# Kernel optimization log

Measured on AMD Instinct MI355X. Metric: run time of the kernel, lower is better.

The kernel has to match this reference:

```python
import jax, jax.numpy as jnp
import numpy as np

WIN_H, WIN_W = 4, 7
WIN = WIN_H * WIN_W  # 28 sample points == feature channels
GRID_OFF = (0.0, 40.0)
SPATIAL_SCALE = 1.0 / 0.4
BN_EPS = 1e-3


def setup_inputs() -> dict:
    key = jax.random.key(0)
    ks = jax.random.split(key, 5)
    B, Cin, H, W = 4, 256, 200, 176
    Cout, N = WIN, 2048
    x = jax.random.normal(ks[0], (B, Cin, H, W), dtype=jnp.float32)
    # boxes [x, y, z, w, l, h, r] in realistic KITTI ranges
    lo = jnp.array([0.0, -40.0, -3.0, 1.5, 3.2, 1.4, -np.pi], jnp.float32)
    hi = jnp.array([70.0, 40.0, 1.0, 2.0, 4.2, 1.8, np.pi], jnp.float32)
    u = jax.random.uniform(ks[1], (B, N, 7), dtype=jnp.float32)
    guided_anchors = lo + u * (hi - lo)
    w1 = jax.random.normal(ks[2], (Cout, Cin, 3, 3), jnp.float32) * 0.02
    gamma = jnp.ones((Cout,), jnp.float32)
    beta = jnp.zeros((Cout,), jnp.float32)
    running_mean = jnp.zeros((Cout,), jnp.float32)
    running_var = jnp.ones((Cout,), jnp.float32)
    w2 = jax.random.normal(ks[3], (Cout, Cout, 1, 1), jnp.float32) * 0.05
    return dict(x=x, guided_anchors=guided_anchors, w1=w1, gamma=gamma,
                beta=beta, running_mean=running_mean, running_var=running_var, w2=w2)


def _convs(x, w1, gamma, beta, mean, var, w2):
    dn = ('NCHW', 'OIHW', 'NCHW')
    y = jax.lax.conv_general_dilated(x, w1, (1, 1), 'SAME', dimension_numbers=dn)
    scale = gamma * jax.lax.rsqrt(var + BN_EPS)
    y = y * scale[:, None, None] + (beta - mean * scale)[:, None, None]  # BN (inference)
    y = jax.nn.relu(y)
    return jax.lax.conv_general_dilated(y, w2, (1, 1), 'SAME', dimension_numbers=dn)


def _gen_sample_grid(box5):
    xg, yg, wg, lg, rg = (box5[:, i] for i in range(5))
    c = jnp.cos(rg)[:, None, None]
    s = jnp.sin(rg)[:, None, None]
    xx = (jnp.linspace(-0.5, 0.5, WIN_H)[None, :] * wg[:, None])[:, :, None]  # (N,4,1)
    yy = (jnp.linspace(-0.5, 0.5, WIN_W)[None, :] * lg[:, None])[:, None, :]  # (N,1,7)
    xpix = xx * c + yy * s + xg[:, None, None]  # (N,4,7)
    ypix = yy * c - xx * s + yg[:, None, None]  # (N,4,7)
    xs = ((jnp.transpose(xpix, (1, 2, 0)) + GRID_OFF[0]) * SPATIAL_SCALE).reshape(WIN, -1)
    ys = ((jnp.transpose(ypix, (1, 2, 0)) + GRID_OFF[1]) * SPATIAL_SCALE).reshape(WIN, -1)
    return xs, ys


def _bilinear_sample(img, xs, ys):
    # img: (C,H,W); xs, ys: (C,N) pixel coords (align_corners=True semantics,
    # zero padding outside) -> (C,N). Channel c samples at grid row c.
    C, H, W = img.shape
    x0 = jnp.floor(xs); y0 = jnp.floor(ys)
    wx = xs - x0; wy = ys - y0
    cidx = jnp.arange(C)[:, None]

    def gather(yf, xf):
        yi = yf.astype(jnp.int32); xi = xf.astype(jnp.int32)
        valid = (yf >= 0) & (yf <= H - 1) & (xf >= 0) & (xf <= W - 1)
        v = img[cidx, jnp.clip(yi, 0, H - 1), jnp.clip(xi, 0, W - 1)]
        return jnp.where(valid, v, 0.0)

    return (gather(y0, x0) * (1 - wx) * (1 - wy)
            + gather(y0, x0 + 1) * wx * (1 - wy)
            + gather(y0 + 1, x0) * (1 - wx) * wy
            + gather(y0 + 1, x0 + 1) * wx * wy)


def reference(x, guided_anchors, w1, gamma, beta, running_mean, running_var, w2):
    feat = _convs(x, w1, gamma, beta, running_mean, running_var, w2)  # (B,28,H,W)
    box5 = guided_anchors[:, :, jnp.array([0, 1, 3, 4, 6])]           # (B,N,5)
    xs, ys = jax.vmap(_gen_sample_grid)(box5)                          # (B,28,N) each
    vals = jax.vmap(_bilinear_sample)(feat, xs, ys)                    # (B,28,N)
    scores = jnp.mean(vals, axis=1)                                    # (B,N)
    return scores.reshape(-1)                                          # (B*N,)
```

## Files before the change

kernel.cpp:

```cpp
#include <hip/hip_runtime.h>
#include <hip/hip_bf16.h>

#define HH 200
#define WW 176
#define CIN 256
#define CO 28
#define BN_EPS 1e-3f

typedef __attribute__((ext_vector_type(8))) short short8;
typedef __attribute__((ext_vector_type(4))) float f32x4;

static __device__ __forceinline__ ushort f2bf(float f) {
    __hip_bfloat16 h = __float2bfloat16(f);
    return __builtin_bit_cast(ushort, h);
}

__global__ void prep_k(const float* __restrict__ w1, const float* __restrict__ gamma,
                       const float* __restrict__ beta, const float* __restrict__ mean,
                       const float* __restrict__ var, ushort* __restrict__ w1b,
                       float* __restrict__ shift)
{
    int idx = blockIdx.x * 256 + threadIdx.x;
    if (idx < CO) {
        float sc = gamma[idx] * rsqrtf(var[idx] + BN_EPS);
        shift[idx] = beta[idx] - mean[idx] * sc;
    }
    if (idx < 8 * 9 * 2 * 64 * 8) {
        int j   = idx & 7;
        int l   = (idx >> 3) & 63;
        int n   = (idx >> 9) & 1;
        int rem = idx >> 10;
        int t   = rem % 9;
        int h   = rem / 9;
        int co = n * 16 + (l & 15);
        int ci = h * 32 + (l >> 4) * 8 + j;
        float v = 0.f;
        if (co < CO) {
            float sc = gamma[co] * rsqrtf(var[co] + BN_EPS);
            v = w1[(co * CIN + ci) * 9 + t] * sc;
        }
        w1b[idx] = f2bf(v);
    }
}

__global__ __launch_bounds__(256, 2) void conv_mfma_k(
    const float* __restrict__ x, const ushort* __restrict__ w1b,
    const float* __restrict__ shift, float* __restrict__ y1)
{
    __shared__ uint4 sbuf[4][768];

    const int tid  = threadIdx.x;
    const int lane = tid & 63;
    const int w    = tid >> 6;
    const int wu   = __builtin_amdgcn_readfirstlane(w);
    const int c_   = lane & 15;
    const int oct  = lane >> 4;

    const int NB = 11 * 25 * 4;
    const int q = NB / 8, r = NB % 8;
    const int bid  = blockIdx.x;
    const int xcd  = bid & 7;
    const int rank = bid >> 3;
    const int tile = (xcd < r ? xcd * (q + 1) : r * (q + 1) + (xcd - r) * q) + rank;

    const int tx  = tile % 11;
    const int rem = tile / 11;
    const int ty  = rem % 25;
    const int b   = rem / 25;
    const int x0  = tx * 16, y0 = ty * 8;

    const float* xb = x + (size_t)b * CIN * HH * WW;

    int  soff[3]; bool sval[3];
#pragma unroll
    for (int it = 0; it < 3; ++it) {
        int p = it * 64 + lane;
        int rr = p / 18, cc = p - rr * 18;
        int gy = y0 + rr - 1, gx = x0 + cc - 1;
        bool v = (gy >= 0) & (gy < HH) & (gx >= 0) & (gx < WW);
        sval[it] = v;
        soff[it] = v ? gy * WW + gx : 0;
    }
    const uint voff0 = (uint)(soff[0] * 4);
    const uint voff1 = (uint)(soff[1] * 4);
    const uint voff2 = (uint)(soff[2] * 4);
    const uint wvoff = (uint)(lane * 16);

    float  xA[24], xB[24];
    short8 wqA[6], wqB[6];

    f32x4 acc[8][2];
#pragma unroll
    for (int m = 0; m < 8; ++m)
#pragma unroll
        for (int n = 0; n < 2; ++n)
            acc[m][n] = (f32x4){0.f, 0.f, 0.f, 0.f};

#define ISSUE24(ch, o, XR)                                                    \
    {                                                                         \
        _Pragma("unroll")                                                     \
        for (int j = 0; j < 8; ++j) {                                         \
            const float* bj = xb + (size_t)((ch) * 32 + (o) * 8 + j) * 35200; \
            asm volatile("global_load_dword %0, %1, %2"                       \
                         : "=v"(XR[0 + j]) : "v"(voff0), "s"(bj));            \
            asm volatile("global_load_dword %0, %1, %2"                       \
                         : "=v"(XR[8 + j]) : "v"(voff1), "s"(bj));            \
            asm volatile("global_load_dword %0, %1, %2"                       \
                         : "=v"(XR[16 + j]) : "v"(voff2), "s"(bj));           \
        }                                                                     \
    }

#define WAITX(N, XR)                                                          \
    asm volatile("s_waitcnt vmcnt(" #N ")"                                    \
        : "+v"(XR[0]), "+v"(XR[1]), "+v"(XR[2]), "+v"(XR[3]), "+v"(XR[4]),    \
          "+v"(XR[5]), "+v"(XR[6]), "+v"(XR[7]), "+v"(XR[8]), "+v"(XR[9]),    \
          "+v"(XR[10]), "+v"(XR[11]));                                        \
    asm volatile("s_waitcnt vmcnt(" #N ")"                                    \
        : "+v"(XR[12]), "+v"(XR[13]), "+v"(XR[14]), "+v"(XR[15]),             \
          "+v"(XR[16]), "+v"(XR[17]), "+v"(XR[18]), "+v"(XR[19]),             \
          "+v"(XR[20]), "+v"(XR[21]), "+v"(XR[22]), "+v"(XR[23]));            \
    __builtin_amdgcn_sched_barrier(0);

#define PACK(XR, o)                                                           \
    {                                                                         \
        _Pragma("unroll")                                                     \
        for (int it = 0; it < 3; ++it) {                                      \
            int p = it * 64 + lane;                                           \
            ushort u[8];                                                      \
            _Pragma("unroll")                                                 \
            for (int j = 0; j < 8; ++j)                                       \
                u[j] = sval[it] ? f2bf(XR[it * 8 + j]) : (ushort)0;           \
            uint4 val;                                                        \
            val.x = (uint)u[0] | ((uint)u[1] << 16);                          \
            val.y = (uint)u[2] | ((uint)u[3] << 16);                          \
            val.z = (uint)u[4] | ((uint)u[5] << 16);                          \
            val.w = (uint)u[6] | ((uint)u[7] << 16);                          \
            sbuf[w][p * 4 + (((o) + (p >> 1)) & 3)] = val;                    \
        }                                                                     \
    }

#define WLOAD6(ch, dx, WQ)                                                    \
    {                                                                         \
        const ushort* wbase = w1b + (size_t)(ch) * 9216;                      \
        _Pragma("unroll")                                                     \
        for (int dy = 0; dy < 3; ++dy) {                                      \
            _Pragma("unroll")                                                 \
            for (int n = 0; n < 2; ++n) {                                     \
                const ushort* bk = wbase + (size_t)((dy * 3 + (dx)) * 2 + n) * 512; \
                asm volatile("global_load_dwordx4 %0, %1, %2"                 \
                             : "=v"(WQ[dy * 2 + n]) : "v"(wvoff), "s"(bk));   \
            }                                                                 \
        }                                                                     \
    }

#define WAITW(N, WQ)                                                          \
    asm volatile("s_waitcnt vmcnt(" #N ")"                                    \
        : "+v"(WQ[0]), "+v"(WQ[1]), "+v"(WQ[2]), "+v"(WQ[3]), "+v"(WQ[4]),    \
          "+v"(WQ[5]));                                                       \
    __builtin_amdgcn_sched_barrier(0);

#define COMP_DX(dx, WQ)                                                       \
    {                                                                         \
        short8 av[10];                                                        \
        _Pragma("unroll")                                                     \
        for (int rr = 0; rr < 10; ++rr) {                                     \
            int p = rr * 18 + c_ + (dx);                                      \
            av[rr] = __builtin_bit_cast(short8,                               \
                sbuf[w][p * 4 + ((oct + (p >> 1)) & 3)]);                     \
        }                                                                     \
        _Pragma("unroll")                                                     \
        for (int dy = 0; dy < 3; ++dy) {                                      \
            _Pragma("unroll")                                                 \
            for (int m = 0; m < 8; ++m) {                                     \
                acc[m][0] = __builtin_amdgcn_mfma_f32_16x16x32_bf16(          \
                    av[m + dy], WQ[dy * 2 + 0], acc[m][0], 0, 0, 0);          \
                acc[m][1] = __builtin_amdgcn_mfma_f32_16x16x32_bf16(          \
                    av[m + dy], WQ[dy * 2 + 1], acc[m][1], 0, 0, 0);          \
            }                                                                 \
        }                                                                     \
    }

#define STAGE(ch)                                                             \
    {                                                                         \
        ISSUE24(ch, 0, xA); ISSUE24(ch, 1, xB);                               \
        WAITX(24, xA) PACK(xA, 0);                                            \
        ISSUE24(ch, 2, xA);                                                   \
        WAITX(24, xB) PACK(xB, 1);                                            \
        ISSUE24(ch, 3, xB);                                                   \
        WAITX(24, xA) PACK(xA, 2);                                            \
        WLOAD6(ch, 0, wqA);                                                   \
        WAITX(6, xB) PACK(xB, 3);                                             \
    }

#define COMPCH(ch)                                                            \
    {                                                                         \
        WLOAD6(ch, 1, wqB);                                                   \
        WAITW(6, wqA) COMP_DX(0, wqA);                                        \
        WLOAD6(ch, 2, wqA);                                                   \
        WAITW(6, wqB) COMP_DX(1, wqB);                                        \
        WAITW(0, wqA) COMP_DX(2, wqA);                                        \
    }

    STAGE(wu)
    COMPCH(wu)
    STAGE(wu + 4)
    COMPCH(wu + 4)

    __syncthreads();
    f32x4* rb = (f32x4*)&sbuf[0][0];
    if (w > 0) {
        int base = (w - 1) * 1024 + lane;
#pragma unroll
        for (int m = 0; m < 8; ++m)
#pragma unroll
            for (int n = 0; n < 2; ++n)
                rb[base + (m * 2 + n) * 64] = acc[m][n];
    }
    __syncthreads();
    if (w == 0) {
        const float s0 = shift[c_];
        const float s1 = (16 + c_ < CO) ? shift[16 + c_] : 0.f;
#pragma unroll
        for (int m = 0; m < 8; ++m) {
            int gy = y0 + m;
#pragma unroll
            for (int n = 0; n < 2; ++n) {
                f32x4 s = acc[m][n];
#pragma unroll
                for (int v = 1; v < 4; ++v)
                    s += rb[(v - 1) * 1024 + (m * 2 + n) * 64 + lane];
                const float sh = n ? s1 : s0;
                const int co = n * 16 + c_;
                if (co < CO) {
#pragma unroll
                    for (int reg = 0; reg < 4; ++reg) {
                        int gx = x0 + oct * 4 + reg;
                        float* yp = y1 + ((size_t)(b * HH + gy) * WW + gx) * CO;
                        float vv = s[reg] + sh;
                        yp[co] = vv > 0.f ? vv : 0.f;
                    }
                }
            }
        }
    }
}

__global__ __launch_bounds__(224) void sample_k(
    const float* __restrict__ y1, const float* __restrict__ ga,
    const float* __restrict__ w2, float* __restrict__ out)
{
    __shared__ float red[224];
    const int lb  = threadIdx.x / CO;
    const int k   = threadIdx.x % CO;
    const int box = blockIdx.x * 8 + lb;
    const int b   = box >> 11;

    const float* ap = ga + (size_t)box * 7;
    float xg = ap[0], yg = ap[1], wg = ap[3], lg = ap[4], rg = ap[6];
    float c = cosf(rg), s = sinf(rg);

    const int i = k / 7, j = k % 7;
    float xx = ((float)i * (1.f / 3.f) - 0.5f) * wg;
    float yy = ((float)j * (1.f / 6.f) - 0.5f) * lg;
    float xs = (xx * c + yy * s + xg) * 2.5f;
    float ys = (yy * c - xx * s + yg + 40.f) * 2.5f;

    float x0 = floorf(xs), y0 = floorf(ys);
    float wx = xs - x0,    wy = ys - y0;

    float w2r[CO];
    const float* w2p = w2 + k * CO;
#pragma unroll
    for (int q = 0; q < 7; ++q) {
        float4 t = ((const float4*)w2p)[q];
        w2r[4*q] = t.x; w2r[4*q+1] = t.y; w2r[4*q+2] = t.z; w2r[4*q+3] = t.w;
    }

    float val = 0.f;
    const float* yb = y1 + (size_t)b * HH * WW * CO;
#pragma unroll
    for (int cor = 0; cor < 4; ++cor) {
        float yf = y0 + (float)(cor >> 1);
        float xf = x0 + (float)(cor & 1);
        float cw = ((cor & 1) ? wx : 1.f - wx) * ((cor >> 1) ? wy : 1.f - wy);
        if (yf >= 0.f && yf <= (float)(HH - 1) && xf >= 0.f && xf <= (float)(WW - 1)) {
            int yi = (int)yf, xi = (int)xf;
            const float* p = yb + ((size_t)yi * WW + xi) * CO;
            float d = 0.f;
#pragma unroll
            for (int q = 0; q < 7; ++q) {
                float4 t = ((const float4*)p)[q];
                d = fmaf(w2r[4*q],   t.x, d);
                d = fmaf(w2r[4*q+1], t.y, d);
                d = fmaf(w2r[4*q+2], t.z, d);
                d = fmaf(w2r[4*q+3], t.w, d);
            }
            val = fmaf(cw, d, val);
        }
    }

    red[threadIdx.x] = val;
    __syncthreads();
    if (k == 0) {
        float sum = 0.f;
#pragma unroll
        for (int q = 0; q < CO; ++q) sum += red[lb * CO + q];
        out[box] = sum * (1.f / 28.f);
    }
}

extern "C" void kernel_launch(void* const* d_in, const int* in_sizes, int n_in,
                              void* d_out, int out_size, void* d_ws, size_t ws_size,
                              hipStream_t stream) {
    const float* x     = (const float*)d_in[0];
    const float* ga    = (const float*)d_in[1];
    const float* w1    = (const float*)d_in[2];
    const float* gamma = (const float*)d_in[3];
    const float* beta  = (const float*)d_in[4];
    const float* mean  = (const float*)d_in[5];
    const float* var   = (const float*)d_in[6];
    const float* w2    = (const float*)d_in[7];
    float* out = (float*)d_out;

    ushort* w1b   = (ushort*)d_ws;
    float*  shift = (float*)((char*)d_ws + 147456);
    float*  y1    = (float*)((char*)d_ws + 147968);

    prep_k<<<(8 * 9 * 2 * 64 * 8 + 255) / 256, 256, 0, stream>>>(
        w1, gamma, beta, mean, var, w1b, shift);

    conv_mfma_k<<<11 * 25 * 4, 256, 0, stream>>>(x, w1b, shift, y1);

    sample_k<<<(4 * 2048) / 8, 224, 0, stream>>>(y1, ga, w2, out);
}
```

Measured before the change: 75.51 us.

## Load conv input tiles with dwordx4 row quads into a padded channel-minor LDS layout

```diff
diff --git a/kernel.cpp b/kernel.cpp
--- a/kernel.cpp
+++ b/kernel.cpp
@@ -47,7 +47,7 @@
     const float* __restrict__ x, const ushort* __restrict__ w1b,
     const float* __restrict__ shift, float* __restrict__ y1)
 {
-    __shared__ uint4 sbuf[4][768];
+    __shared__ ushort sA[4][9600];
 
     const int tid  = threadIdx.x;
     const int lane = tid & 63;
@@ -55,6 +55,9 @@
     const int wu   = __builtin_amdgcn_readfirstlane(w);
     const int c_   = lane & 15;
     const int oct  = lane >> 4;
+    const int jl   = lane & 7;
+    const int p    = (lane >> 3) & 1;
+    const int ci   = oct * 8 + jl;
 
     const int NB = 11 * 25 * 4;
     const int q = NB / 8, r = NB % 8;
@@ -69,105 +72,94 @@
     const int b   = rem / 25;
     const int x0  = tx * 16, y0 = ty * 8;
 
-    const float* xb = x + (size_t)b * CIN * HH * WW;
-
-    int  soff[3]; bool sval[3];
-#pragma unroll
-    for (int it = 0; it < 3; ++it) {
-        int p = it * 64 + lane;
-        int rr = p / 18, cc = p - rr * 18;
-        int gy = y0 + rr - 1, gx = x0 + cc - 1;
-        bool v = (gy >= 0) & (gy < HH) & (gx >= 0) & (gx < WW);
-        sval[it] = v;
-        soff[it] = v ? gy * WW + gx : 0;
-    }
-    const uint voff0 = (uint)(soff[0] * 4);
-    const uint voff1 = (uint)(soff[1] * 4);
-    const uint voff2 = (uint)(soff[2] * 4);
+    const char* xbb = (const char*)(x + (size_t)b * CIN * HH * WW);
     const uint wvoff = (uint)(lane * 16);
 
-    float  xA[24], xB[24];
+    auto geovoff = [&](int i) -> uint {
+        int qu  = 2 * i + p;
+        int row = qu / 6, qc = qu - row * 6;
+        int gy  = y0 + row - 1;
+        int gyc = gy < 0 ? 0 : (gy > HH - 1 ? HH - 1 : gy);
+        int gx0 = x0 - 4 + qc * 4;
+        int gx0c = gx0 < 0 ? 0 : (gx0 > WW - 4 ? WW - 4 : gx0);
+        return (uint)((ci * (HH * WW) + gyc * WW + gx0c) * 4);
+    };
+    auto packone = [&](int i, f32x4 v) {
+        int qu  = 2 * i + p;
+        int row = qu / 6, qc = qu - row * 6;
+        int gy  = y0 + row - 1;
+        bool yv = (gy >= 0) & (gy < HH);
+        int gx0 = x0 - 4 + qc * 4;
+        ushort* dst = &sA[w][(qu * 4) * 40 + ci];
+#pragma unroll
+        for (int k = 0; k < 4; ++k) {
+            bool valid = yv & (gx0 + k >= 0) & (gx0 + k < WW);
+            dst[k * 40] = valid ? f2bf(v[k]) : (ushort)0;
+        }
+    };
+
+    f32x4  sa[10], sb[10], sc[10];
     short8 wqA[6], wqB[6];
-
-    f32x4 acc[8][2];
+    f32x4  acc[8][2];
 #pragma unroll
     for (int m = 0; m < 8; ++m)
 #pragma unroll
         for (int n = 0; n < 2; ++n)
             acc[m][n] = (f32x4){0.f, 0.f, 0.f, 0.f};
 
-#define ISSUE24(ch, o, XR)                                                    \
-    {                                                                         \
-        _Pragma("unroll")                                                     \
-        for (int j = 0; j < 8; ++j) {                                         \
-            const float* bj = xb + (size_t)((ch) * 32 + (o) * 8 + j) * 35200; \
-            asm volatile("global_load_dword %0, %1, %2"                       \
-                         : "=v"(XR[0 + j]) : "v"(voff0), "s"(bj));            \
-            asm volatile("global_load_dword %0, %1, %2"                       \
-                         : "=v"(XR[8 + j]) : "v"(voff1), "s"(bj));            \
-            asm volatile("global_load_dword %0, %1, %2"                       \
-                         : "=v"(XR[16 + j]) : "v"(voff2), "s"(bj));           \
+#define SBAR __builtin_amdgcn_sched_barrier(0)
+
+#define XISS(ch, SET, I0)                                                     \
+    {                                                                         \
+        const char* bj = xbb + (size_t)(ch) * 4505600;                        \
+        _Pragma("unroll")                                                     \
+        for (int i = 0; i < 10; ++i) {                                        \
+            uint vo = geovoff(i + (I0));                                      \
+            asm volatile("global_load_dwordx4 %0, %1, %2"                     \
+                         : "=v"(SET[i]) : "v"(vo), "s"(bj));                  \
         }                                                                     \
     }
 
-#define WAITX(N, XR)                                                          \
+#define VWX(N, SET)                                                           \
     asm volatile("s_waitcnt vmcnt(" #N ")"                                    \
-        : "+v"(XR[0]), "+v"(XR[1]), "+v"(XR[2]), "+v"(XR[3]), "+v"(XR[4]),    \
-          "+v"(XR[5]), "+v"(XR[6]), "+v"(XR[7]), "+v"(XR[8]), "+v"(XR[9]),    \
-          "+v"(XR[10]), "+v"(XR[11]));                                        \
-    asm volatile("s_waitcnt vmcnt(" #N ")"                                    \
-        : "+v"(XR[12]), "+v"(XR[13]), "+v"(XR[14]), "+v"(XR[15]),             \
-          "+v"(XR[16]), "+v"(XR[17]), "+v"(XR[18]), "+v"(XR[19]),             \
-          "+v"(XR[20]), "+v"(XR[21]), "+v"(XR[22]), "+v"(XR[23]));            \
-    __builtin_amdgcn_sched_barrier(0);
-
-#define PACK(XR, o)                                                           \
-    {                                                                         \
-        _Pragma("unroll")                                                     \
-        for (int it = 0; it < 3; ++it) {                                      \
-            int p = it * 64 + lane;                                           \
-            ushort u[8];                                                      \
-            _Pragma("unroll")                                                 \
-            for (int j = 0; j < 8; ++j)                                       \
-                u[j] = sval[it] ? f2bf(XR[it * 8 + j]) : (ushort)0;           \
-            uint4 val;                                                        \
-            val.x = (uint)u[0] | ((uint)u[1] << 16);                          \
-            val.y = (uint)u[2] | ((uint)u[3] << 16);                          \
-            val.z = (uint)u[4] | ((uint)u[5] << 16);                          \
-            val.w = (uint)u[6] | ((uint)u[7] << 16);                          \
-            sbuf[w][p * 4 + (((o) + (p >> 1)) & 3)] = val;                    \
-        }                                                                     \
-    }
-
-#define WLOAD6(ch, dx, WQ)                                                    \
-    {                                                                         \
-        const ushort* wbase = w1b + (size_t)(ch) * 9216;                      \
+        : "+v"(SET[0]), "+v"(SET[1]), "+v"(SET[2]), "+v"(SET[3]),             \
+          "+v"(SET[4]), "+v"(SET[5]), "+v"(SET[6]), "+v"(SET[7]),             \
+          "+v"(SET[8]), "+v"(SET[9]));                                        \
+    SBAR;
+
+#define PACK10(SET, I0)                                                       \
+    {                                                                         \
+        _Pragma("unroll")                                                     \
+        for (int i = 0; i < 10; ++i) packone(i + (I0), SET[i]);               \
+    }
+
+#define WISS(ch, dx, WQ)                                                      \
+    {                                                                         \
+        const ushort* wb = w1b + (size_t)(ch) * 9216;                         \
         _Pragma("unroll")                                                     \
         for (int dy = 0; dy < 3; ++dy) {                                      \
             _Pragma("unroll")                                                 \
             for (int n = 0; n < 2; ++n) {                                     \
-                const ushort* bk = wbase + (size_t)((dy * 3 + (dx)) * 2 + n) * 512; \
+                const ushort* bk = wb + (size_t)((dy * 3 + (dx)) * 2 + n) * 512; \
                 asm volatile("global_load_dwordx4 %0, %1, %2"                 \
                              : "=v"(WQ[dy * 2 + n]) : "v"(wvoff), "s"(bk));   \
             }                                                                 \
         }                                                                     \
     }
 
-#define WAITW(N, WQ)                                                          \
+#define VWW(N, WQ)                                                            \
     asm volatile("s_waitcnt vmcnt(" #N ")"                                    \
         : "+v"(WQ[0]), "+v"(WQ[1]), "+v"(WQ[2]), "+v"(WQ[3]), "+v"(WQ[4]),    \
           "+v"(WQ[5]));                                                       \
-    __builtin_amdgcn_sched_barrier(0);
+    SBAR;
 
 #define COMP_DX(dx, WQ)                                                       \
     {                                                                         \
+        const ushort* swp = &sA[w][0];                                        \
         short8 av[10];                                                        \
         _Pragma("unroll")                                                     \
-        for (int rr = 0; rr < 10; ++rr) {                                     \
-            int p = rr * 18 + c_ + (dx);                                      \
-            av[rr] = __builtin_bit_cast(short8,                               \
-                sbuf[w][p * 4 + ((oct + (p >> 1)) & 3)]);                     \
-        }                                                                     \
+        for (int rr = 0; rr < 10; ++rr)                                       \
+            av[rr] = *(const short8*)&swp[(rr * 24 + c_ + (dx) + 3) * 40 + oct * 8]; \
         _Pragma("unroll")                                                     \
         for (int dy = 0; dy < 3; ++dy) {                                      \
             _Pragma("unroll")                                                 \
@@ -180,34 +172,26 @@
         }                                                                     \
     }
 
-#define STAGE(ch)                                                             \
-    {                                                                         \
-        ISSUE24(ch, 0, xA); ISSUE24(ch, 1, xB);                               \
-        WAITX(24, xA) PACK(xA, 0);                                            \
-        ISSUE24(ch, 2, xA);                                                   \
-        WAITX(24, xB) PACK(xB, 1);                                            \
-        ISSUE24(ch, 3, xB);                                                   \
-        WAITX(24, xA) PACK(xA, 2);                                            \
-        WLOAD6(ch, 0, wqA);                                                   \
-        WAITX(6, xB) PACK(xB, 3);                                             \
-    }
-
-#define COMPCH(ch)                                                            \
-    {                                                                         \
-        WLOAD6(ch, 1, wqB);                                                   \
-        WAITW(6, wqA) COMP_DX(0, wqA);                                        \
-        WLOAD6(ch, 2, wqA);                                                   \
-        WAITW(6, wqB) COMP_DX(1, wqB);                                        \
-        WAITW(0, wqA) COMP_DX(2, wqA);                                        \
-    }
-
-    STAGE(wu)
-    COMPCH(wu)
-    STAGE(wu + 4)
-    COMPCH(wu + 4)
+#define CHUNK(ch)                                                             \
+    {                                                                         \
+        XISS(ch, sa, 0) XISS(ch, sb, 10)                                      \
+        VWX(10, sa) PACK10(sa, 0)                                             \
+        XISS(ch, sc, 20)                                                      \
+        VWX(10, sb) PACK10(sb, 10)                                            \
+        WISS(ch, 0, wqA)                                                      \
+        VWX(6, sc) PACK10(sc, 20)                                             \
+        WISS(ch, 1, wqB)                                                      \
+        VWW(6, wqA) COMP_DX(0, wqA)                                           \
+        WISS(ch, 2, wqA)                                                      \
+        VWW(6, wqB) COMP_DX(1, wqB)                                           \
+        VWW(0, wqA) COMP_DX(2, wqA)                                           \
+    }
+
+    CHUNK(wu)
+    CHUNK(wu + 4)
 
     __syncthreads();
-    f32x4* rb = (f32x4*)&sbuf[0][0];
+    f32x4* rb = (f32x4*)&sA[0][0];
     if (w > 0) {
         int base = (w - 1) * 1024 + lane;
 #pragma unroll
@@ -285,11 +269,11 @@
         float cw = ((cor & 1) ? wx : 1.f - wx) * ((cor >> 1) ? wy : 1.f - wy);
         if (yf >= 0.f && yf <= (float)(HH - 1) && xf >= 0.f && xf <= (float)(WW - 1)) {
             int yi = (int)yf, xi = (int)xf;
-            const float* p = yb + ((size_t)yi * WW + xi) * CO;
+            const float* pp = yb + ((size_t)yi * WW + xi) * CO;
             float d = 0.f;
 #pragma unroll
             for (int q = 0; q < 7; ++q) {
-                float4 t = ((const float4*)p)[q];
+                float4 t = ((const float4*)pp)[q];
                 d = fmaf(w2r[4*q],   t.x, d);
                 d = fmaf(w2r[4*q+1], t.y, d);
                 d = fmaf(w2r[4*q+2], t.z, d);
```

New measurement: 84.50 us. 11.9% more time.
